# Kernel tuning notes

Measured on AMD Instinct MI355X. Metric: run time of the kernel, lower is better.

## Reference

```python
import jax, jax.numpy as jnp
import numpy as np

N, E, G = 50000, 800000, 512          # nodes, edges, graphs in batch
DIN, DH, H, DOUT = 128, 128, 2, 128   # dim_in, dim_h, heads, dim_out
NEG_SLOPE = 0.2
EPS_BN = 1e-5


def setup_inputs():
    key = jax.random.key(0)
    ks = jax.random.split(key, 12)
    def glorot(k, shape, fan):
        return (jax.random.normal(k, shape, jnp.float32) / np.float32(np.sqrt(fan)))
    return dict(
        x=jax.random.normal(ks[0], (N, DIN), jnp.float32),
        edge_index=jax.random.randint(ks[1], (2, E), 0, N, dtype=jnp.int32),
        batch=jnp.sort(jax.random.randint(ks[2], (N,), 0, G, dtype=jnp.int32)),
        Wl1=glorot(ks[3], (DIN, H * DH), DIN),
        Wr1=glorot(ks[4], (DIN, H * DH), DIN),
        att1=glorot(ks[5], (H, DH), DH),
        b1=jnp.zeros((H * DH,), jnp.float32),
        gamma=jnp.ones((H * DH,), jnp.float32),
        beta=jnp.zeros((H * DH,), jnp.float32),
        Wl2=glorot(ks[6], (H * DH, DOUT), H * DH),
        Wr2=glorot(ks[7], (H * DH, DOUT), H * DH),
        att2=glorot(ks[8], (1, DOUT), DOUT),
        b2=jnp.zeros((DOUT,), jnp.float32),
        Wlin=glorot(ks[9], (DOUT, 2), DOUT),
        blin=jnp.zeros((2,), jnp.float32),
    )


def gatv2_conv(x, src, dst, Wl, Wr, att, bias, heads, dh, n):
    # x: [n, F]; src/dst: [Etot] (self-loops already appended)
    xl = (x @ Wl).reshape(n, heads, dh)  # source transform (messages)
    xr = (x @ Wr).reshape(n, heads, dh)  # target transform
    m = xl[src] + xr[dst]                             # [Etot, H, dh]
    e = jnp.einsum('ehd,hd->eh', jax.nn.leaky_relu(m, NEG_SLOPE), att)  # [Etot, H]
    # softmax over incoming edges of each target node
    emax = jax.ops.segment_max(e, dst, num_segments=n)
    ex = jnp.exp(e - emax[dst])
    denom = jax.ops.segment_sum(ex, dst, num_segments=n)
    alpha = ex / (denom[dst] + 1e-16)                 # [Etot, H]
    out = jax.ops.segment_sum(xl[src] * alpha[:, :, None], dst, num_segments=n)
    return out.reshape(n, heads * dh) + bias


def reference(x, edge_index, batch, Wl1, Wr1, att1, b1, gamma, beta,
              Wl2, Wr2, att2, b2, Wlin, blin):
    loops = jnp.arange(N, dtype=edge_index.dtype)
    src = jnp.concatenate([edge_index[0], loops])
    dst = jnp.concatenate([edge_index[1], loops])

    h = gatv2_conv(x, src, dst, Wl1, Wr1, att1, b1, H, DH, N)   # [N, H*DH]
    h = jax.nn.elu(h)
    # BatchNorm over node dimension (training-mode batch stats)
    mu = h.mean(axis=0)
    var = h.var(axis=0)
    h = (h - mu) * jax.lax.rsqrt(var + EPS_BN) * gamma + beta
    # dropout p=0 -> identity
    h = gatv2_conv(h, src, dst, Wl2, Wr2, att2, b2, 1, DOUT, N)  # [N, DOUT]

    # global mean pool per graph
    s = jax.ops.segment_sum(h, batch, num_segments=G)
    cnt = jax.ops.segment_sum(jnp.ones((N,), h.dtype), batch, num_segments=G)
    pooled = s / jnp.maximum(cnt, 1.0)[:, None]                  # [G, DOUT]
    return pooled @ Wlin + blin                                  # [G, 2]
```

## Files before the change

kernel.cpp:

```cpp
#include <hip/hip_runtime.h>


#define DIN 128
#define F1 256
#define F2 128
#define NEG_SLOPE 0.2f

typedef unsigned short u16;
typedef __attribute__((ext_vector_type(8))) short short8;
typedef __attribute__((ext_vector_type(4))) float floatx4;
typedef __attribute__((ext_vector_type(2))) float f32x2;

__device__ __forceinline__ float bf2f(u16 u) {
  return __uint_as_float(((unsigned int)u) << 16);
}
__device__ __forceinline__ u16 f2bf(float f) {
  unsigned int x = __float_as_uint(f);
  return (u16)((x + 0x7fffu + ((x >> 16) & 1u)) >> 16);
}
__device__ __forceinline__ void load8(const u16* p, float (&f)[8]) {
  short8 v = *(const short8*)p;
#pragma unroll
  for (int k = 0; k < 8; k++) f[k] = bf2f((u16)v[k]);
}

__device__ __forceinline__ f32x2 bf2x(unsigned int u) {
  f32x2 r;
  r.x = __uint_as_float(u << 16);
  r.y = __uint_as_float(u & 0xffff0000u);
  return r;
}
__device__ __forceinline__ f32x2 pk_add(f32x2 a, f32x2 b) {
  f32x2 d;
  asm("v_pk_add_f32 %0, %1, %2" : "=v"(d) : "v"(a), "v"(b));
  return d;
}
__device__ __forceinline__ f32x2 pk_fma(f32x2 a, f32x2 b, f32x2 c) {
  f32x2 d;
  asm("v_pk_fma_f32 %0, %1, %2, %3" : "=v"(d) : "v"(a), "v"(b), "v"(c));
  return d;
}
__device__ __forceinline__ f32x2 pk_abs(f32x2 a) {
  f32x2 r;
  r.x = __uint_as_float(__float_as_uint(a.x) & 0x7fffffffu);
  r.y = __uint_as_float(__float_as_uint(a.y) & 0x7fffffffu);
  return r;
}

template <int CTRL>
__device__ __forceinline__ float dppadd(float s) {
  int t = __builtin_amdgcn_update_dpp(0, __float_as_int(s), CTRL, 0xF, 0xF, false);
  return s + __int_as_float(t);
}

struct PTab { const void* src[8]; int off[9]; };
__global__ __launch_bounds__(256) void k_convert_all(
    const void* __restrict__ xsrc, u16* __restrict__ xb, int n4, int nxb,
    PTab t, u16* __restrict__ pb, int ptotal, int npb,
    const void* __restrict__ Wl1s, const void* __restrict__ Wr1s,
    const void* __restrict__ Wl2s, const void* __restrict__ Wr2s,
    u16* __restrict__ Wl1t, u16* __restrict__ Wr1t,
    u16* __restrict__ Wl2t, u16* __restrict__ Wr2t,
    int* __restrict__ zbase, int zn, int* __restrict__ flag) {
  __shared__ int flagS;
  int tid = threadIdx.x;
  if (tid < 64) {
    int cnt = 0;
#pragma unroll
    for (int i = 0; i < 2; ++i) {
      u16 v = ((const u16*)xsrc)[2 * (tid + 64 * i)];
      int e = (v >> 7) & 0xFF;
      if (e >= 115 && e <= 130) cnt++;
    }
#pragma unroll
    for (int m = 1; m <= 32; m <<= 1) cnt += __shfl_xor(cnt, m, 64);
    if (tid == 0) flagS = (cnt < 64) ? 1 : 0;
  }
  __syncthreads();
  const int fl = flagS;
  if (blockIdx.x == 0 && tid == 0) *flag = fl;

  int b = blockIdx.x;
  if (b < nxb) {
    int i = b * 256 + tid;
    if (i >= n4) return;
    if (fl) {
      float4 a = ((const float4*)xsrc)[i];
      ushort4 o;
      o.x = f2bf(a.x); o.y = f2bf(a.y); o.z = f2bf(a.z); o.w = f2bf(a.w);
      ((ushort4*)xb)[i] = o;
    } else {
      ((ulong1*)xb)[i] = ((const ulong1*)xsrc)[i];
    }
    return;
  }
  b -= nxb;
  if (b < npb) {
    int i = b * 256 + tid;
    if (i >= ptotal) return;
    int s = 0;
#pragma unroll
    for (int k = 1; k < 8; k++) s += (i >= t.off[k]);
    int local = i - t.off[s];
    pb[i] = fl ? f2bf(((const float*)t.src[s])[local]) : ((const u16*)t.src[s])[local];
    return;
  }
  b -= npb;
  if (b < 512) {
    int seg = b >> 7;
    int i = (b & 127) * 256 + tid;
    const void* s; u16* d; int NL, sh;
    if      (seg == 0) { s = Wl1s; d = Wl1t; NL = 256; sh = 7; }
    else if (seg == 1) { s = Wr1s; d = Wr1t; NL = 256; sh = 7; }
    else if (seg == 2) { s = Wl2s; d = Wl2t; NL = 128; sh = 8; }
    else               { s = Wr2s; d = Wr2t; NL = 128; sh = 8; }
    int n = i >> sh, k = i & ((1 << sh) - 1);
    int si = k * NL + n;
    d[i] = fl ? f2bf(((const float*)s)[si]) : ((const u16*)s)[si];
    return;
  }
  b -= 512;
  int i = b * 256 + tid;
  if (i < zn) zbase[i] = 0;
}

__global__ void k_hist(const int* __restrict__ ei, int* __restrict__ hist,
                       int E, int Etot) {
  int e = blockIdx.x * 256 + threadIdx.x;
  if (e >= Etot) return;
  int dst = (e < E) ? ei[E + e] : (e - E);
  atomicAdd(&hist[dst], 1);
}

__global__ void k_scan(const int* __restrict__ hist, int* __restrict__ rowptr,
                       int* __restrict__ cursor, unsigned long long* __restrict__ pstate,
                       int* __restrict__ ctr, int n, int Etot) {
  __shared__ int tmp[256];
  __shared__ int bidS, offS;
  int t = threadIdx.x;
  if (t == 0) bidS = atomicAdd(ctr, 1);
  __syncthreads();
  int bid = bidS;
  int gid = bid * 256 + t;
  int v = (gid < n) ? hist[gid] : 0;
  tmp[t] = v;
  __syncthreads();
  for (int off = 1; off < 256; off <<= 1) {
    int add = (t >= off) ? tmp[t - off] : 0;
    __syncthreads();
    tmp[t] += add;
    __syncthreads();
  }
  if (t == 0) {
    int total = tmp[255];
    unsigned long long st =
        ((unsigned long long)(bid == 0 ? 2 : 1) << 32) | (unsigned)total;
    atomicExch(&pstate[bid], st);
    int off = 0;
    if (bid > 0) {
      int b = bid - 1;
      while (true) {
        unsigned long long s;
        do { s = atomicAdd(&pstate[b], 0ULL); } while ((s >> 32) == 0);
        off += (int)(unsigned)s;
        if ((s >> 32) == 2) break;
        b--;
      }
      atomicExch(&pstate[bid],
                 ((unsigned long long)2 << 32) | (unsigned)(off + total));
    }
    offS = off;
  }
  __syncthreads();
  int off = offS;
  if (gid < n) {
    int ex = off + tmp[t] - v;
    rowptr[gid] = ex;
    cursor[gid] = ex;
  }
  if (gid == 0) rowptr[n] = Etot;
}

__global__ void k_scatter(const int* __restrict__ ei, int* __restrict__ cursor,
                          int* __restrict__ ssrc, int E, int Etot) {
  int e = blockIdx.x * 256 + threadIdx.x;
  if (e >= Etot) return;
  int src, dst;
  if (e < E) { src = ei[e]; dst = ei[E + e]; }
  else       { src = e - E; dst = e - E; }
  int pos = atomicAdd(&cursor[dst], 1);
  ssrc[pos] = src;
}

template<int K, bool RB>
__global__ __launch_bounds__(256) void k_gemm(
    const u16* __restrict__ A, const u16* __restrict__ Blt, const u16* __restrict__ Brt,
    int NL, u16* __restrict__ Cl, u16* __restrict__ Cr, int M,
    const float* __restrict__ rbias) {
  const int tid = threadIdx.x;
  const int m0 = blockIdx.x * 64;
  const int n0g = blockIdx.y * 64;
  const u16* Bt; u16* C; int col0;
  if (n0g < NL) { Bt = Blt; C = Cl; col0 = n0g; }
  else          { Bt = Brt; C = Cr; col0 = n0g - NL; }

  const int wave = tid >> 6, lane = tid & 63;
  const int wm = wave >> 1, wn = wave & 1;
  const int quad = lane >> 4, l16 = lane & 15;

  floatx4 acc[2][2] = {};
#pragma unroll
  for (int k0 = 0; k0 < K; k0 += 32) {
    short8 af[2], bfr[2];
#pragma unroll
    for (int mt = 0; mt < 2; mt++) {
      int row = m0 + wm * 32 + mt * 16 + l16;
      if (row > M - 1) row = M - 1;
      af[mt] = *(const short8*)(A + (size_t)row * K + k0 + quad * 8);
    }
#pragma unroll
    for (int nt = 0; nt < 2; nt++) {
      int nn = col0 + wn * 32 + nt * 16 + l16;
      bfr[nt] = *(const short8*)(Bt + (size_t)nn * K + k0 + quad * 8);
    }
#pragma unroll
    for (int mt = 0; mt < 2; mt++)
#pragma unroll
      for (int nt = 0; nt < 2; nt++)
        acc[mt][nt] = __builtin_amdgcn_mfma_f32_16x16x32_bf16(af[mt], bfr[nt], acc[mt][nt], 0, 0, 0);
  }

#pragma unroll
  for (int mt = 0; mt < 2; mt++)
#pragma unroll
    for (int nt = 0; nt < 2; nt++) {
      float rb = 0.f;
      if (RB) rb = rbias[n0g + wn * 32 + nt * 16 + l16];
#pragma unroll
      for (int r = 0; r < 4; r++) {
        int row = m0 + wm * 32 + mt * 16 + quad * 4 + r;
        if (row < M) {
          int col = col0 + wn * 32 + nt * 16 + l16;
          C[(size_t)row * NL + col] = f2bf(acc[mt][nt][r] + rb);
        }
      }
    }
}

template<int CPL, int MODE>
__global__ __launch_bounds__(256) void k_agg(
    const u16* __restrict__ xl, const u16* __restrict__ xr,
    const u16* __restrict__ att, const u16* __restrict__ bias,
    const int* __restrict__ rowptr, const int* __restrict__ ssrc,
    void* __restrict__ outv, int n) {
  constexpr int F = CPL * 16;
  constexpr int NV = CPL / 8;
  constexpr int NP = CPL / 2;
  int wave = threadIdx.x >> 6, lane = threadIdx.x & 63;
  int node = blockIdx.x * 4 + wave;
  if (node >= n) return;
  const int q = lane >> 4, l = lane & 15;
  const int ch0 = l * CPL;

  f32x2 xr2[NP], a06[NP], a04[NP], acc2[NP];
  {
    const unsigned int* xru = (const unsigned int*)(xr + (size_t)node * F + ch0);
    const unsigned int* atu = (const unsigned int*)(att + ch0);
#pragma unroll
    for (int p = 0; p < NP; p++) {
      xr2[p] = bf2x(xru[p]);
      f32x2 a = bf2x(atu[p]);
      a06[p].x = 0.6f * a.x; a06[p].y = 0.6f * a.y;
      a04[p].x = 0.4f * a.x; a04[p].y = 0.4f * a.y;
      acc2[p].x = 0.f;       acc2[p].y = 0.f;
    }
  }

  const int jb = __builtin_amdgcn_readfirstlane(rowptr[node]);
  const int je = __builtin_amdgcn_readfirstlane(rowptr[node + 1]);
  float l_run = 0.f;

  int jj = jb + q;
  int scur = ssrc[jj < je ? jj : je - 1];
  int jn = jb + 4 + q;
  int snxt = ssrc[jn < je ? jn : je - 1];
  uint4 cur[NV], nxt[NV];
#pragma unroll
  for (int v = 0; v < NV; v++)
    cur[v] = *(const uint4*)(xl + (size_t)scur * F + ch0 + v * 8);

  for (int j = jb; j < je; j += 4) {
#pragma unroll
    for (int v = 0; v < NV; v++)
      nxt[v] = *(const uint4*)(xl + (size_t)snxt * F + ch0 + v * 8);
    int jnn = j + 8 + q;
    snxt = ssrc[jnn < je ? jnn : je - 1];

    f32x2 xl2[NP];
    f32x2 s2; s2.x = 0.f; s2.y = 0.f;
#pragma unroll
    for (int v = 0; v < NV; v++) {
      unsigned int dw[4] = {cur[v].x, cur[v].y, cur[v].z, cur[v].w};
#pragma unroll
      for (int k = 0; k < 4; k++) {
        const int p = v * 4 + k;
        f32x2 xv = bf2x(dw[k]);
        f32x2 m  = pk_add(xv, xr2[p]);
        f32x2 am = pk_abs(m);
        s2 = pk_fma(a06[p], m, s2);
        s2 = pk_fma(a04[p], am, s2);
        xl2[p] = xv;
      }
    }

    float s = s2.x + s2.y;
    s = dppadd<0xB1>(s);
    s = dppadd<0x4E>(s);
    s = dppadd<0x141>(s);
    if (CPL == 8) s = dppadd<0x140>(s);

    float pe = (j + q < je) ? __expf(fminf(s, 80.f)) : 0.f;
    l_run += pe;
    f32x2 p2; p2.x = pe; p2.y = pe;
#pragma unroll
    for (int p = 0; p < NP; p++) acc2[p] = pk_fma(p2, xl2[p], acc2[p]);

#pragma unroll
    for (int v = 0; v < NV; v++) cur[v] = nxt[v];
  }

#pragma unroll
  for (int p = 0; p < NP; p++) {
    acc2[p].x += __shfl_xor(acc2[p].x, 16, 64);
    acc2[p].x += __shfl_xor(acc2[p].x, 32, 64);
    acc2[p].y += __shfl_xor(acc2[p].y, 16, 64);
    acc2[p].y += __shfl_xor(acc2[p].y, 32, 64);
  }
  l_run += __shfl_xor(l_run, 16, 64);
  l_run += __shfl_xor(l_run, 32, 64);

  if (q == 0) {
    float inv = 1.f / (l_run + 1e-16f);
    const unsigned int* bu = (const unsigned int*)(bias + ch0);
    if (MODE == 0) {
#pragma unroll
      for (int v = 0; v < NV; v++) {
        short8 o;
#pragma unroll
        for (int k = 0; k < 4; k++) {
          const int p = v * 4 + k;
          f32x2 b = bf2x(bu[p]);
          float t0 = acc2[p].x * inv + b.x;
          float t1 = acc2[p].y * inv + b.y;
          t0 = t0 > 0.f ? t0 : (__expf(t0) - 1.f);
          t1 = t1 > 0.f ? t1 : (__expf(t1) - 1.f);
          o[k * 2]     = (short)f2bf(t0);
          o[k * 2 + 1] = (short)f2bf(t1);
        }
        *(short8*)((u16*)outv + (size_t)node * F + ch0 + v * 8) = o;
      }
    } else {
#pragma unroll
      for (int v = 0; v < NV; v++) {
        float w[8];
#pragma unroll
        for (int k = 0; k < 4; k++) {
          const int p = v * 4 + k;
          f32x2 b = bf2x(bu[p]);
          w[k * 2]     = acc2[p].x * inv + b.x;
          w[k * 2 + 1] = acc2[p].y * inv + b.y;
        }
        float* op = (float*)outv + (size_t)node * F + ch0 + v * 8;
        *(float4*)op = make_float4(w[0], w[1], w[2], w[3]);
        *(float4*)(op + 4) = make_float4(w[4], w[5], w[6], w[7]);
      }
    }
  }
}

__global__ __launch_bounds__(256) void k_stats(
    const u16* __restrict__ h, float* __restrict__ gsum,
    float* __restrict__ gsumsq, int n) {
  __shared__ float smS[8][256], smQ[8][256];
  int t = threadIdx.x;
  int rg = t >> 5, cl = t & 31;
  int ch0 = cl * 8;
  float s[8] = {}, q[8] = {};
  for (int r = blockIdx.x * 8 + rg; r < n; r += gridDim.x * 8) {
    float v[8];
    load8(h + (size_t)r * F1 + ch0, v);
#pragma unroll
    for (int k = 0; k < 8; k++) { s[k] += v[k]; q[k] += v[k] * v[k]; }
  }
#pragma unroll
  for (int k = 0; k < 8; k++) { smS[rg][ch0 + k] = s[k]; smQ[rg][ch0 + k] = q[k]; }
  __syncthreads();
  float ts = 0.f, tq = 0.f;
#pragma unroll
  for (int g = 0; g < 8; g++) { ts += smS[g][t]; tq += smQ[g][t]; }
  atomicAdd(&gsum[t], ts);
  atomicAdd(&gsumsq[t], tq);
}

__global__ __launch_bounds__(256) void k_foldbn(
    const float* __restrict__ gsum, const float* __restrict__ gsumsq,
    const u16* __restrict__ gamma, const u16* __restrict__ beta,
    u16* __restrict__ Wl2t, u16* __restrict__ Wr2t,
    float* __restrict__ rbias, float invn) {
  __shared__ float red[8];
  int t = threadIdx.x, n = blockIdx.x;
  float mu = gsum[t] * invn;
  float var = gsumsq[t] * invn - mu * mu;
  float a = bf2f(gamma[t]) * rsqrtf(fmaxf(var, 0.f) + 1e-5f);
  float b = bf2f(beta[t]) - mu * a;
  float wl = bf2f(Wl2t[n * 256 + t]);
  float wr = bf2f(Wr2t[n * 256 + t]);
  float sl = b * wl, sr = b * wr;
  Wl2t[n * 256 + t] = f2bf(a * wl);
  Wr2t[n * 256 + t] = f2bf(a * wr);
#pragma unroll
  for (int m = 1; m <= 32; m <<= 1) {
    sl += __shfl_xor(sl, m, 64);
    sr += __shfl_xor(sr, m, 64);
  }
  int wave = t >> 6, lane = t & 63;
  if (lane == 0) { red[wave] = sl; red[4 + wave] = sr; }
  __syncthreads();
  if (t == 0) rbias[n] = red[0] + red[1] + red[2] + red[3];
  if (t == 1) rbias[128 + n] = red[4] + red[5] + red[6] + red[7];
}

__device__ __forceinline__ int lowerb(const int* __restrict__ a, int n, int key) {
  int lo = 0, hi = n;
  while (lo < hi) { int m = (lo + hi) >> 1; if (a[m] < key) lo = m + 1; else hi = m; }
  return lo;
}

__global__ __launch_bounds__(256) void k_poolfinal(
    const float* __restrict__ h2, const int* __restrict__ batch,
    const u16* __restrict__ Wlin, const u16* __restrict__ blin,
    void* __restrict__ out, const int* __restrict__ flag, int G, int N) {
  __shared__ float sm[4][128];
  int g = blockIdx.x;
  int wave = threadIdx.x >> 6, lane = threadIdx.x & 63;
  int jb = lowerb(batch, N, g);
  int je = lowerb(batch, N, g + 1);
  int ch = lane * 2;
  float c0 = 0.f, c1 = 0.f;
  for (int r = jb + wave; r < je; r += 4) {
    float2 v = *(const float2*)(h2 + (size_t)r * F2 + ch);
    c0 += v.x; c1 += v.y;
  }
  sm[wave][ch] = c0;
  sm[wave][ch + 1] = c1;
  __syncthreads();
  if (wave == 0) {
    c0 = sm[0][ch] + sm[1][ch] + sm[2][ch] + sm[3][ch];
    c1 = sm[0][ch + 1] + sm[1][ch + 1] + sm[2][ch + 1] + sm[3][ch + 1];
    float cf = fmaxf((float)(je - jb), 1.f);
    c0 /= cf; c1 /= cf;
    float s0 = c0 * bf2f(Wlin[ch * 2 + 0]) + c1 * bf2f(Wlin[(ch + 1) * 2 + 0]);
    float s1 = c0 * bf2f(Wlin[ch * 2 + 1]) + c1 * bf2f(Wlin[(ch + 1) * 2 + 1]);
#pragma unroll
    for (int m = 1; m <= 32; m <<= 1) {
      s0 += __shfl_xor(s0, m, 64);
      s1 += __shfl_xor(s1, m, 64);
    }
    if (lane == 0) {
      float o0 = s0 + bf2f(blin[0]);
      float o1 = s1 + bf2f(blin[1]);
      if (*flag) {
        ((float*)out)[g * 2 + 0] = o0;
        ((float*)out)[g * 2 + 1] = o1;
      } else {
        ((u16*)out)[g * 2 + 0] = f2bf(o0);
        ((u16*)out)[g * 2 + 1] = f2bf(o1);
      }
    }
  }
}

extern "C" void kernel_launch(void* const* d_in, const int* in_sizes, int n_in,
                              void* d_out, int out_size, void* d_ws, size_t ws_size,
                              hipStream_t stream) {
  const int* ei    = (const int*)d_in[1];
  const int* batch = (const int*)d_in[2];

  const int N = in_sizes[0] / DIN;
  const int E = in_sizes[1] / 2;
  const int G = out_size / 2;
  const int Etot = E + N;

  char* p = (char*)d_ws;
  auto alloc = [&](size_t bytes) {
    char* r = p;
    p += (bytes + 255) & ~(size_t)255;
    return r;
  };
  int*  flag     = (int*)alloc(256);
  int*  hist     = (int*)alloc((size_t)N * 4);
  float* gsum    = (float*)alloc(1024);
  float* gsumsq  = (float*)alloc(1024);
  unsigned long long* pstate = (unsigned long long*)alloc(2048);
  int*  ctr      = (int*)alloc(256);
  int   zn       = (int)(((char*)ctr + 256) - (char*)hist) / 4;
  int*  rowptr   = (int*)alloc((size_t)(N + 1) * 4);
  int*  cursor   = (int*)alloc((size_t)N * 4);
  float* rbias   = (float*)alloc(256 * 4);
  int*  ssrc     = (int*)alloc((size_t)Etot * 4);
  u16*  xb       = (u16*)alloc((size_t)N * DIN * 2);
  u16*  pb       = (u16*)alloc(4096);
  u16*  Wl1t     = (u16*)alloc(DIN * F1 * 2);
  u16*  Wr1t     = (u16*)alloc(DIN * F1 * 2);
  u16*  Wl2t     = (u16*)alloc(F1 * F2 * 2);
  u16*  Wr2t     = (u16*)alloc(F1 * F2 * 2);
  u16*  regionA  = (u16*)alloc((size_t)N * F1 * 2);
  u16*  regionB  = (u16*)alloc((size_t)N * F1 * 2);
  u16*  regionC  = (u16*)alloc((size_t)N * F1 * 2);

  u16*  xl1  = regionA;
  u16*  xr1  = regionB;
  u16*  helu = regionC;
  u16*  xl2  = regionB;
  u16*  xr2  = regionB + (size_t)N * F2;
  float* h2  = (float*)regionA;

  const int pidx[8] = {5, 6, 7, 8, 11, 12, 13, 14};
  PTab tab;
  int accum = 0;
  for (int i = 0; i < 8; i++) {
    tab.src[i] = d_in[pidx[i]];
    tab.off[i] = accum;
    accum += in_sizes[pidx[i]];
  }
  tab.off[8] = accum;
  int n4 = in_sizes[0] / 4;
  int nxb = (n4 + 255) / 256;
  int npb = (accum + 255) / 256;
  int nzb = (zn + 255) / 256;
  k_convert_all<<<nxb + npb + 512 + nzb, 256, 0, stream>>>(
      d_in[0], xb, n4, nxb, tab, pb, accum, npb,
      d_in[3], d_in[4], d_in[9], d_in[10], Wl1t, Wr1t, Wl2t, Wr2t,
      hist, zn, flag);
  u16 *pAtt1 = pb + tab.off[0], *pB1 = pb + tab.off[1], *pGamma = pb + tab.off[2],
      *pBeta = pb + tab.off[3], *pAtt2 = pb + tab.off[4], *pB2 = pb + tab.off[5],
      *pWlin = pb + tab.off[6], *pBlin = pb + tab.off[7];

  const int eb = (Etot + 255) / 256;
  const int sb = (N + 255) / 256;

  k_hist<<<eb, 256, 0, stream>>>(ei, hist, E, Etot);
  k_scan<<<sb, 256, 0, stream>>>(hist, rowptr, cursor, pstate, ctr, N, Etot);
  k_scatter<<<eb, 256, 0, stream>>>(ei, cursor, ssrc, E, Etot);

  dim3 g1((N + 63) / 64, (2 * F1) / 64);
  k_gemm<DIN, false><<<g1, 256, 0, stream>>>(xb, Wl1t, Wr1t, F1, xl1, xr1, N, nullptr);

  k_agg<16, 0><<<(N + 3) / 4, 256, 0, stream>>>(xl1, xr1, pAtt1, pB1, rowptr, ssrc, helu, N);

  k_stats<<<256, 256, 0, stream>>>(helu, gsum, gsumsq, N);
  k_foldbn<<<128, 256, 0, stream>>>(gsum, gsumsq, pGamma, pBeta, Wl2t, Wr2t, rbias,
                                    1.0f / (float)N);

  dim3 g2((N + 63) / 64, (2 * F2) / 64);
  k_gemm<F1, true><<<g2, 256, 0, stream>>>(helu, Wl2t, Wr2t, F2, xl2, xr2, N, rbias);

  k_agg<8, 1><<<(N + 3) / 4, 256, 0, stream>>>(xl2, xr2, pAtt2, pB2, rowptr, ssrc, h2, N);

  k_poolfinal<<<G, 256, 0, stream>>>(h2, batch, pWlin, pBlin, d_out, flag, G, N);
}
```

Before: 448.6 us.

## Double-buffer edge gathers in aggregation and fold leaky-relu into one FMA

The aggregation loop now keeps two named register buffers and handles two 4-edge slots per iteration, so gathers of later source rows are issued earlier and there is no register copy between cur and nxt. The leaky-relu attention term is rewritten as 0.6*a*(m + (2/3)|m|), which needs one fewer packed FMA and drops the a04 register array. The deeper prefetch raises register pressure and adds a tail path for an odd number of slots.

```diff
diff --git a/kernel.cpp b/kernel.cpp
--- a/kernel.cpp
+++ b/kernel.cpp
@@ -262,7 +262,7 @@
   const int q = lane >> 4, l = lane & 15;
   const int ch0 = l * CPL;
 
-  f32x2 xr2[NP], a06[NP], a04[NP], acc2[NP];
+  f32x2 xr2[NP], a06[NP], acc2[NP];
   {
     const unsigned int* xru = (const unsigned int*)(xr + (size_t)node * F + ch0);
     const unsigned int* atu = (const unsigned int*)(att + ch0);
@@ -271,63 +271,69 @@
       xr2[p] = bf2x(xru[p]);
       f32x2 a = bf2x(atu[p]);
       a06[p].x = 0.6f * a.x; a06[p].y = 0.6f * a.y;
-      a04[p].x = 0.4f * a.x; a04[p].y = 0.4f * a.y;
       acc2[p].x = 0.f;       acc2[p].y = 0.f;
     }
   }
+  f32x2 c23; c23.x = 2.0f / 3.0f; c23.y = 2.0f / 3.0f;
 
   const int jb = __builtin_amdgcn_readfirstlane(rowptr[node]);
   const int je = __builtin_amdgcn_readfirstlane(rowptr[node + 1]);
+  const int jec = je - 1;
   float l_run = 0.f;
 
-  int jj = jb + q;
-  int scur = ssrc[jj < je ? jj : je - 1];
-  int jn = jb + 4 + q;
-  int snxt = ssrc[jn < je ? jn : je - 1];
-  uint4 cur[NV], nxt[NV];
-#pragma unroll
-  for (int v = 0; v < NV; v++)
-    cur[v] = *(const uint4*)(xl + (size_t)scur * F + ch0 + v * 8);
-
-  for (int j = jb; j < je; j += 4) {
+  auto cidx = [&](int j) -> int { return j < jec ? j : jec; };
+
+  uint4 bufA[NV], bufB[NV];
+  auto REFILL = [&](uint4 (&buf)[NV], int srow) {
 #pragma unroll
     for (int v = 0; v < NV; v++)
-      nxt[v] = *(const uint4*)(xl + (size_t)snxt * F + ch0 + v * 8);
-    int jnn = j + 8 + q;
-    snxt = ssrc[jnn < je ? jnn : je - 1];
-
+      buf[v] = *(const uint4*)(xl + (size_t)srow * F + ch0 + v * 8);
+  };
+
+  auto SLOT = [&](uint4 (&buf)[NV], int jbase) {
     f32x2 xl2[NP];
     f32x2 s2; s2.x = 0.f; s2.y = 0.f;
 #pragma unroll
     for (int v = 0; v < NV; v++) {
-      unsigned int dw[4] = {cur[v].x, cur[v].y, cur[v].z, cur[v].w};
+      unsigned int dw[4] = {buf[v].x, buf[v].y, buf[v].z, buf[v].w};
 #pragma unroll
       for (int k = 0; k < 4; k++) {
         const int p = v * 4 + k;
         f32x2 xv = bf2x(dw[k]);
         f32x2 m  = pk_add(xv, xr2[p]);
         f32x2 am = pk_abs(m);
-        s2 = pk_fma(a06[p], m, s2);
-        s2 = pk_fma(a04[p], am, s2);
+        f32x2 t  = pk_fma(am, c23, m);
+        s2 = pk_fma(a06[p], t, s2);
         xl2[p] = xv;
       }
     }
-
     float s = s2.x + s2.y;
     s = dppadd<0xB1>(s);
     s = dppadd<0x4E>(s);
     s = dppadd<0x141>(s);
     if (CPL == 8) s = dppadd<0x140>(s);
-
-    float pe = (j + q < je) ? __expf(fminf(s, 80.f)) : 0.f;
+    float pe = (jbase + q < je) ? __expf(fminf(s, 80.f)) : 0.f;
     l_run += pe;
     f32x2 p2; p2.x = pe; p2.y = pe;
 #pragma unroll
     for (int p = 0; p < NP; p++) acc2[p] = pk_fma(p2, xl2[p], acc2[p]);
-
-#pragma unroll
-    for (int v = 0; v < NV; v++) cur[v] = nxt[v];
-  }
+  };
+
+  REFILL(bufA, ssrc[cidx(jb + q)]);
+  REFILL(bufB, ssrc[cidx(jb + 4 + q)]);
+  int sA2 = ssrc[cidx(jb + 8 + q)];
+  int sB2 = ssrc[cidx(jb + 12 + q)];
+
+  int j = jb;
+  for (; j + 4 < je; j += 8) {
+    SLOT(bufA, j);
+    REFILL(bufA, sA2);
+    SLOT(bufB, j + 4);
+    REFILL(bufB, sB2);
+    sA2 = ssrc[cidx(j + 16 + q)];
+    sB2 = ssrc[cidx(j + 20 + q)];
+  }
+  if (j < je) SLOT(bufA, j);
 
 #pragma unroll
   for (int p = 0; p < NP; p++) {
```

New measurement: 434.7 us (median of 2 runs). -3.1%, faster.
